# Kernel tuning notes

Hardware: AMD Instinct MI355X
Metric: run time of the kernel (lower is better)

The kernel has to match this reference:

```python
import jax, jax.numpy as jnp
import numpy as np
import math

B, N, FEAT, H, NONGT, M, POS = 16, 1024, 768, 8, 20, 10, 64
DG = FEAT // H  # per-head dim = 96
NEG = -9e15


def setup_inputs() -> dict:
    key = jax.random.key(0)
    ks = jax.random.split(key, 14)
    s = 0.02
    return dict(
        roi_feat=jax.random.normal(ks[0], (B, N, FEAT), jnp.float32),
        adj_matrix=jax.random.randint(ks[1], (B, N, NONGT), 0, 2).astype(jnp.int32),
        position_embedding=jax.random.uniform(ks[2], (B, N, NONGT, POS), jnp.float32),
        label_biases_att=jax.random.normal(ks[3], (B, N, NONGT), jnp.float32) * 0.1,
        aux_feat=jax.random.normal(ks[4], (B, 1, FEAT), jnp.float32),
        Wq=jax.random.normal(ks[5], (FEAT, FEAT), jnp.float32) * s,
        bq=jnp.zeros((FEAT,), jnp.float32),
        Wk=jax.random.normal(ks[6], (FEAT, FEAT), jnp.float32) * s,
        bk=jnp.zeros((FEAT,), jnp.float32),
        Wpos=jax.random.normal(ks[7], (POS, H), jnp.float32) * s,
        bpos=jnp.zeros((H,), jnp.float32),
        m_k=jax.random.normal(ks[8], (1, M, FEAT), jnp.float32) * (1.0 / FEAT / H),
        m_v=jax.random.normal(ks[9], (1, M, FEAT), jnp.float32) * (1.0 / M),
        Wout=jax.random.normal(ks[10], (H, DG, FEAT), jnp.float32) * s,  # grouped 1x1 conv: per-head [DG, FEAT]
        bout=jnp.zeros((FEAT,), jnp.float32),
    )


def reference(roi_feat, adj_matrix, position_embedding, label_biases_att, aux_feat,
              Wq, bq, Wk, bk, Wpos, bpos, m_k, m_v, Wout, bout):
    b, n, f = roi_feat.shape
    nongt = min(NONGT, n)
    nongt_feat = roi_feat[:, :nongt]                               # [B,nongt,F]

    q = (roi_feat @ Wq + bq).reshape(b, n, H, DG)                  # [B,N,H,DG]
    scale_m = math.sqrt(f / H)
    mk = scale_m * m_k * aux_feat                                  # [B,M,F] (broadcast)
    mv = scale_m * m_v * aux_feat                                  # [B,M,F]
    k = jnp.concatenate([nongt_feat @ Wk + bk, mk], axis=1)        # [B,K,F], K=nongt+M
    v = jnp.concatenate([nongt_feat, mv], axis=1)                  # [B,K,F]
    kk = k.reshape(b, nongt + M, H, DG)

    # scaled QK^T -> [B,N,H,K]
    aff = jnp.einsum('bnhd,bkhd->bnhk', q, kk) / math.sqrt(DG)

    # geometric position bias: log(max(relu(fc(pos)), 1e-6)) on first nongt keys
    pos = jax.nn.relu(position_embedding @ Wpos + bpos)            # [B,N,nongt,H]
    bias = jnp.log(jnp.maximum(pos, 1e-6))
    aff_n = aff[:, :, :, :nongt] + jnp.transpose(bias, (0, 1, 3, 2))

    # adjacency mask + label bias on first nongt keys
    mask = (adj_matrix > 0)[:, :, None, :]                         # [B,N,1,nongt]
    aff_n = jnp.where(mask, aff_n, NEG) + label_biases_att[:, :, None, :]

    weighted = jnp.concatenate([aff_n, aff[:, :, :, nongt:]], axis=-1)
    p = jax.nn.softmax(weighted, axis=-1)                          # [B,N,H,K]

    out_t = jnp.einsum('bnhk,bkf->bnhf', p, v)                     # [B,N,H,F]
    # weight-normed grouped 1x1 conv == per-head linear F -> DG, concat over heads
    out = jnp.einsum('bnhf,hgf->bnhg', out_t, Wout).reshape(b, n, f) + bout
    return out
```

## Files before the change

kernel.cpp:

```cpp
#include <hip/hip_runtime.h>
#include <hip/hip_bf16.h>
#include <cstdint>

typedef __bf16 bf16;
typedef __bf16 bf16x4 __attribute__((ext_vector_type(4)));
typedef __bf16 bf16x8 __attribute__((ext_vector_type(8)));
typedef float f32x4 __attribute__((ext_vector_type(4)));

#define B_ 16
#define N_ 1024
#define FEAT_ 768
#define H_ 8
#define NONGT_ 20
#define M_ 10
#define POS_ 64
#define DG_ 96
#define KTOT_ 30
#define KPAD_ 32
#define ROWS_ (B_*N_)
#define SCALE_M 9.797958971132712f
#define INV_SQRT_DG 0.10206207261596575f
#define NEG_ -9.0e15f

__device__ __forceinline__ void gload16(const void* g, void* lds) {
  __builtin_amdgcn_global_load_lds(
      (const __attribute__((address_space(1))) unsigned int*)g,
      (__attribute__((address_space(3))) unsigned int*)lds, 16, 0, 0);
}

__device__ __forceinline__ bf16x8 cvt8(float4 a, float4 b) {
  bf16x8 o;
  o[0]=(bf16)a.x; o[1]=(bf16)a.y; o[2]=(bf16)a.z; o[3]=(bf16)a.w;
  o[4]=(bf16)b.x; o[5]=(bf16)b.y; o[6]=(bf16)b.z; o[7]=(bf16)b.w;
  return o;
}

__global__ void prep_kernel(const float* __restrict__ Wq, const float* __restrict__ Wk,
                            const float* __restrict__ Wout, const float* __restrict__ roi,
                            const float* __restrict__ aux, const float* __restrict__ m_v,
                            const float* __restrict__ m_k,
                            bf16* __restrict__ Wq_t, bf16* __restrict__ Wk_t,
                            bf16* __restrict__ Whi, bf16* __restrict__ Wlo,
                            bf16* __restrict__ Vbf, bf16* __restrict__ kbuf,
                            bf16* __restrict__ Abf)
{
  int idx = blockIdx.x * blockDim.x + threadIdx.x;
  int stride = gridDim.x * blockDim.x;
  for (int i = idx; i < FEAT_*FEAT_; i += stride) {
    int n = i / FEAT_, k = i % FEAT_;
    Wq_t[i] = (bf16)Wq[k*FEAT_ + n];
    Wk_t[i] = (bf16)Wk[k*FEAT_ + n];
    float w = Wout[i];
    bf16 hi = (bf16)w;
    Whi[i] = hi;
    Wlo[i] = (bf16)(w - (float)hi);
  }
  for (int i = idx; i < B_*KPAD_*FEAT_; i += stride) {
    int f = i % FEAT_;
    int r = (i / FEAT_) % KPAD_;
    int b = i / (FEAT_*KPAD_);
    float v;
    if (r < NONGT_)      v = roi[((size_t)b*N_ + r)*FEAT_ + f];
    else if (r < KTOT_)  v = SCALE_M * m_v[(r-NONGT_)*FEAT_ + f] * aux[b*FEAT_ + f];
    else                 v = 0.f;
    Vbf[i] = (bf16)v;
  }
  for (int i = idx; i < B_*12*FEAT_; i += stride) {
    int f = i % FEAT_;
    int rr = (i / FEAT_) % 12;
    int b = i / (FEAT_*12);
    float v = (rr < M_) ? SCALE_M * m_k[rr*FEAT_ + f] * aux[b*FEAT_ + f] : 0.f;
    kbuf[((size_t)b*KPAD_ + NONGT_ + rr)*FEAT_ + f] = (bf16)v;
  }
  const int total8 = ROWS_*FEAT_/8;
  for (int i = idx; i < total8; i += stride) {
    const float4* p = (const float4*)(roi + (size_t)i*8);
    *(bf16x8*)(Abf + (size_t)i*8) = cvt8(p[0], p[1]);
  }
}

__global__ __launch_bounds__(256, 2) void gemm_fused_kernel(
    const bf16* __restrict__ A, const bf16* __restrict__ Wq_t,
    const float* __restrict__ bq, bf16* __restrict__ qbuf,
    const bf16* __restrict__ Wk_t, const bf16* __restrict__ Vbf,
    const bf16* __restrict__ Whi, const bf16* __restrict__ Wlo,
    const float* __restrict__ bk, bf16* __restrict__ kbuf,
    bf16* __restrict__ vwT_hi, bf16* __restrict__ vwT_lo)
{
  __shared__ __align__(16) bf16 sA[128*32];
  __shared__ __align__(16) bf16 sB[128*32];
  const int tid = threadIdx.x;
  const int w = tid >> 6, l = tid & 63;
  const int bx = blockIdx.x;
  const int fr = l & 15, fq = l >> 4, fko = fq << 3;

  if (bx < 768) {
    const int x = bx & 7, j = bx >> 3;
    const int mbase = (x + 8*(j/6)) * 128;
    const int nbase = (j % 6) * 128;
    const int wr = w >> 1, wc = w & 1;
    const int srow = tid >> 2;
    const int scol = (tid & 3) << 3;
    const bf16* Ag0 = A + (size_t)(mbase + srow)*FEAT_ + scol;
    const bf16* Ag1 = Ag0 + (size_t)64*FEAT_;
    const bf16* Bg0 = Wq_t + (size_t)(nbase + srow)*FEAT_ + scol;
    const bf16* Bg1 = Bg0 + (size_t)64*FEAT_;
    bf16* ldsA0 = sA + w*512;
    bf16* ldsA1 = sA + 2048 + w*512;
    bf16* ldsB0 = sB + w*512;
    bf16* ldsB1 = sB + 2048 + w*512;
    f32x4 acc[4][4] = {};
    for (int kt = 0; kt < FEAT_/32; ++kt) {
      __syncthreads();
      gload16(Ag0 + kt*32, ldsA0);
      gload16(Ag1 + kt*32, ldsA1);
      gload16(Bg0 + kt*32, ldsB0);
      gload16(Bg1 + kt*32, ldsB1);
      __syncthreads();
      bf16x8 af[4], bff[4];
      #pragma unroll
      for (int m = 0; m < 4; ++m)
        af[m] = *(const bf16x8*)(sA + (wr*64 + m*16 + fr)*32 + fko);
      #pragma unroll
      for (int n = 0; n < 4; ++n)
        bff[n] = *(const bf16x8*)(sB + (wc*64 + n*16 + fr)*32 + fko);
      #pragma unroll
      for (int m = 0; m < 4; ++m) {
        #pragma unroll
        for (int n = 0; n < 4; ++n)
          acc[m][n] = __builtin_amdgcn_mfma_f32_16x16x32_bf16(af[m], bff[n], acc[m][n], 0, 0, 0);
      }
    }
    #pragma unroll
    for (int n = 0; n < 4; ++n) {
      const int col = nbase + wc*64 + n*16 + fr;
      const float bv = bq[col];
      #pragma unroll
      for (int m = 0; m < 4; ++m) {
        const int row = mbase + wr*64 + m*16 + fq*4;
        #pragma unroll
        for (int r = 0; r < 4; ++r)
          qbuf[(size_t)(row + r)*FEAT_ + col] = (bf16)(acc[m][n][r] + bv);
      }
    }
  } else {
    const int widx = (bx - 768)*4 + w;
    const int cbase = (widx % 48) * 16;
    const int by = widx / 48;
    f32x4 acc = {};
    if (by < 32) {
      const bf16* Ap = A + ((size_t)(by >> 1)*N_ + (by & 1)*16 + fr)*FEAT_ + fko;
      const bf16* Bp = Wk_t + (size_t)(cbase + fr)*FEAT_ + fko;
      #pragma unroll
      for (int kt = 0; kt < FEAT_/32; ++kt) {
        bf16x8 a = *(const bf16x8*)(Ap + kt*32);
        bf16x8 b = *(const bf16x8*)(Bp + kt*32);
        acc = __builtin_amdgcn_mfma_f32_16x16x32_bf16(a, b, acc, 0, 0, 0);
      }
      const float bv = bk[cbase + fr];
      #pragma unroll
      for (int r = 0; r < 4; ++r) {
        const int rl = (by & 1)*16 + fq*4 + r;
        if (rl < NONGT_)
          kbuf[((size_t)(by >> 1)*KPAD_ + rl)*FEAT_ + cbase + fr] = (bf16)(acc[r] + bv);
      }
    } else {
      const int rt = by - 32;
      const bf16* Ap = Vbf + ((size_t)rt*16 + fr)*FEAT_ + fko;
      const bf16* B1 = Whi + (size_t)(cbase + fr)*FEAT_ + fko;
      const bf16* B2 = Wlo + (size_t)(cbase + fr)*FEAT_ + fko;
      f32x4 acc2 = {};
      #pragma unroll
      for (int kt = 0; kt < FEAT_/32; ++kt) {
        bf16x8 a = *(const bf16x8*)(Ap + kt*32);
        acc  = __builtin_amdgcn_mfma_f32_16x16x32_bf16(a, *(const bf16x8*)(B1 + kt*32), acc,  0, 0, 0);
        acc2 = __builtin_amdgcn_mfma_f32_16x16x32_bf16(a, *(const bf16x8*)(B2 + kt*32), acc2, 0, 0, 0);
      }
      #pragma unroll
      for (int r = 0; r < 4; ++r) {
        const int grow = rt*16 + fq*4 + r;
        const int b = grow >> 5, key = grow & 31;
        float vv = acc[r] + acc2[r];
        bf16 vh = (bf16)vv;
        size_t addr = ((size_t)b*FEAT_ + cbase + fr)*KPAD_ + key;
        vwT_hi[addr] = vh;
        vwT_lo[addr] = (bf16)(vv - (float)vh);
      }
    }
  }
}

__global__ __launch_bounds__(64, 4) void posbias_kernel(
    const float* __restrict__ pe, const float* __restrict__ Wpos,
    const float* __restrict__ bpos, float* __restrict__ posb)
{
  __shared__ __align__(16) float spe[NONGT_*68];
  __shared__ __align__(16) float swpT[H_*68];
  __shared__ float sbp[H_];
  const int row = blockIdx.x;
  const int l = threadIdx.x;
  const float* per = pe + (size_t)row*NONGT_*POS_;
  for (int i = l; i < NONGT_*POS_; i += 64) spe[(i >> 6)*68 + (i & 63)] = per[i];
  for (int i = l; i < POS_*H_; i += 64) swpT[(i & 7)*68 + (i >> 3)] = Wpos[i];
  if (l < H_) sbp[l] = bpos[l];
  __syncthreads();
  #pragma unroll
  for (int t = 0; t < 3; ++t) {
    int idx = t*64 + l;
    if (idx < NONGT_*H_) {
      int j = idx >> 3, h = idx & 7;
      float s = sbp[h];
      const float4* a4 = (const float4*)(spe + j*68);
      const float4* b4 = (const float4*)(swpT + h*68);
      #pragma unroll
      for (int p4 = 0; p4 < 16; ++p4) {
        float4 a = a4[p4], bv = b4[p4];
        s += a.x*bv.x + a.y*bv.y + a.z*bv.z + a.w*bv.w;
      }
      s = fmaxf(s, 0.f);
      posb[(size_t)row*160 + h*20 + j] = __logf(fmaxf(s, 1e-6f));
    }
  }
}

__global__ __launch_bounds__(256, 4) void attn_kernel(
    const bf16* __restrict__ qbuf, const bf16* __restrict__ kbuf,
    const bf16* __restrict__ vwT_hi, const bf16* __restrict__ vwT_lo,
    const float* __restrict__ posb, const int* __restrict__ adj,
    const float* __restrict__ lb, const float* __restrict__ bout,
    float* __restrict__ out)
{
  __shared__ __align__(16) bf16 sph[H_*16*40];
  __shared__ __align__(16) bf16 spl[H_*16*40];
  const int tid = threadIdx.x;
  const int w = tid >> 6, l = tid & 63;
  const int fr = l & 15, fq = l >> 4, fko = fq << 3;
  const int row0 = blockIdx.x * 16;
  const int b = blockIdx.y;
  const size_t rabs = (size_t)b*N_ + row0 + fr;

  #pragma unroll
  for (int hi2 = 0; hi2 < 2; ++hi2) {
    const int h = w*2 + hi2;
    const bf16* kp = kbuf + (size_t)b*KPAD_*FEAT_ + h*DG_ + fko;
    const bf16* qp = qbuf + rabs*FEAT_ + h*DG_ + fko;
    f32x4 acc0 = {}, acc1 = {};
    #pragma unroll
    for (int kt = 0; kt < 3; ++kt) {
      bf16x8 qa = *(const bf16x8*)(qp + kt*32);
      bf16x8 k0 = *(const bf16x8*)(kp + (size_t)fr*FEAT_ + kt*32);
      bf16x8 k1 = *(const bf16x8*)(kp + (size_t)(16 + fr)*FEAT_ + kt*32);
      acc0 = __builtin_amdgcn_mfma_f32_16x16x32_bf16(k0, qa, acc0, 0, 0, 0);
      acc1 = __builtin_amdgcn_mfma_f32_16x16x32_bf16(k1, qa, acc1, 0, 0, 0);
    }
    const float* pbr = posb + rabs*160 + h*20;
    const int*   adjr = adj + rabs*20;
    const float* lbr  = lb  + rabs*20;
    float lg[2][4];
    #pragma unroll
    for (int r = 0; r < 4; ++r) {
      int j0 = fq*4 + r;
      float v0 = acc0[r] * INV_SQRT_DG;
      v0 = (adjr[j0] > 0 ? v0 + pbr[j0] : NEG_) + lbr[j0];
      lg[0][r] = v0;
      int j1 = 16 + fq*4 + r;
      float v1 = acc1[r] * INV_SQRT_DG;
      if (j1 < NONGT_)      v1 = (adjr[j1] > 0 ? v1 + pbr[j1] : NEG_) + lbr[j1];
      else if (j1 >= KTOT_) v1 = -3.0e38f;
      lg[1][r] = v1;
    }
    float m = lg[0][0];
    #pragma unroll
    for (int jt = 0; jt < 2; ++jt)
      #pragma unroll
      for (int r = 0; r < 4; ++r) m = fmaxf(m, lg[jt][r]);
    m = fmaxf(m, __shfl_xor(m, 16));
    m = fmaxf(m, __shfl_xor(m, 32));
    float s = 0.f;
    float e[2][4];
    #pragma unroll
    for (int jt = 0; jt < 2; ++jt)
      #pragma unroll
      for (int r = 0; r < 4; ++r) { e[jt][r] = __expf(lg[jt][r] - m); s += e[jt][r]; }
    s += __shfl_xor(s, 16);
    s += __shfl_xor(s, 32);
    const float inv = 1.f / s;
    #pragma unroll
    for (int jt = 0; jt < 2; ++jt) {
      bf16x4 ph, pl;
      #pragma unroll
      for (int r = 0; r < 4; ++r) {
        float p = e[jt][r] * inv;
        ph[r] = (bf16)p;
        pl[r] = (bf16)(p - (float)ph[r]);
      }
      const int off = (h*16 + fr)*40 + jt*16 + fq*4;
      *(bf16x4*)(sph + off) = ph;
      *(bf16x4*)(spl + off) = pl;
    }
    bf16x8 pa_h = *(const bf16x8*)(sph + (h*16 + fr)*40 + fko);
    bf16x8 pa_l = *(const bf16x8*)(spl + (h*16 + fr)*40 + fko);
    #pragma unroll
    for (int ct = 0; ct < 6; ++ct) {
      const int col = h*DG_ + ct*16 + fr;
      const size_t vaddr = ((size_t)b*FEAT_ + col)*KPAD_ + fko;
      bf16x8 vh = *(const bf16x8*)(vwT_hi + vaddr);
      bf16x8 vl = *(const bf16x8*)(vwT_lo + vaddr);
      f32x4 o = {};
      o = __builtin_amdgcn_mfma_f32_16x16x32_bf16(pa_h, vh, o, 0, 0, 0);
      o = __builtin_amdgcn_mfma_f32_16x16x32_bf16(pa_h, vl, o, 0, 0, 0);
      o = __builtin_amdgcn_mfma_f32_16x16x32_bf16(pa_l, vh, o, 0, 0, 0);
      const float bv = bout[col];
      #pragma unroll
      for (int r = 0; r < 4; ++r)
        out[((size_t)b*N_ + row0 + fq*4 + r)*FEAT_ + col] = o[r] + bv;
    }
  }
}

extern "C" void kernel_launch(void* const* d_in, const int* in_sizes, int n_in,
                              void* d_out, int out_size, void* d_ws, size_t ws_size,
                              hipStream_t stream) {
  const float* roi  = (const float*)d_in[0];
  const int*   adj  = (const int*)  d_in[1];
  const float* pe   = (const float*)d_in[2];
  const float* lb   = (const float*)d_in[3];
  const float* aux  = (const float*)d_in[4];
  const float* Wq   = (const float*)d_in[5];
  const float* bq   = (const float*)d_in[6];
  const float* Wk   = (const float*)d_in[7];
  const float* bk   = (const float*)d_in[8];
  const float* Wpos = (const float*)d_in[9];
  const float* bpos = (const float*)d_in[10];
  const float* m_k  = (const float*)d_in[11];
  const float* m_v  = (const float*)d_in[12];
  const float* Wout = (const float*)d_in[13];
  const float* bout = (const float*)d_in[14];
  float* out = (float*)d_out;

  char* pw = (char*)d_ws;
  auto carve = [&](size_t bytes) -> void* {
    void* r = pw; pw += (bytes + 255) & ~(size_t)255; return r;
  };
  bf16*  Abf    = (bf16*) carve((size_t)ROWS_*FEAT_*2);
  bf16*  qbuf   = (bf16*) carve((size_t)ROWS_*FEAT_*2);
  bf16*  Wq_t   = (bf16*) carve((size_t)FEAT_*FEAT_*2);
  bf16*  Wk_t   = (bf16*) carve((size_t)FEAT_*FEAT_*2);
  bf16*  Whi    = (bf16*) carve((size_t)FEAT_*FEAT_*2);
  bf16*  Wlo    = (bf16*) carve((size_t)FEAT_*FEAT_*2);
  bf16*  Vbf    = (bf16*) carve((size_t)B_*KPAD_*FEAT_*2);
  bf16*  kbuf   = (bf16*) carve((size_t)B_*KPAD_*FEAT_*2);
  bf16*  vwT_hi = (bf16*) carve((size_t)B_*FEAT_*KPAD_*2);
  bf16*  vwT_lo = (bf16*) carve((size_t)B_*FEAT_*KPAD_*2);
  float* posb   = (float*)carve((size_t)ROWS_*160*4);

  posbias_kernel<<<dim3(16384), dim3(64), 0, stream>>>(pe, Wpos, bpos, posb);
  prep_kernel<<<dim3(2048), dim3(256), 0, stream>>>(Wq, Wk, Wout, roi, aux, m_v, m_k,
                                                    Wq_t, Wk_t, Whi, Wlo, Vbf, kbuf, Abf);
  gemm_fused_kernel<<<dim3(1536), dim3(256), 0, stream>>>(Abf, Wq_t, bq, qbuf,
                                                          Wk_t, Vbf, Whi, Wlo, bk, kbuf,
                                                          vwT_hi, vwT_lo);
  attn_kernel<<<dim3(64, 16), dim3(256), 0, stream>>>(qbuf, kbuf, vwT_hi, vwT_lo,
                                                      posb, adj, lb, bout, out);
}
```

Baseline: 133.1 us.

## Fuse fp32-to-bf16 conversion of roi into GEMM with double-buffered LDS pipeline

Drops the separate pass that converted roi_feat to a bf16 copy. The Q and K GEMMs now read fp32 roi directly and convert in registers, saving a full write and re-read of a 25 MB buffer. The Q GEMM main loop is restructured into a double-buffered LDS pipeline: the next tile's A values are prefetched into registers and its B values via global_load_lds while the current tile's MFMAs run, leaving one barrier per iteration. The Wq/Wk transposes in prep now read coalesced and write strided, and the prep grid is halved. In exchange the GEMM reads twice as many bytes for A and doubles its LDS use, which may reduce occupancy.

Result: faster. 127.6 us (-4.2%).

```diff
diff --git a/kernel.cpp b/kernel.cpp
--- a/kernel.cpp
+++ b/kernel.cpp
@@ -41,15 +41,15 @@
                             const float* __restrict__ m_k,
                             bf16* __restrict__ Wq_t, bf16* __restrict__ Wk_t,
                             bf16* __restrict__ Whi, bf16* __restrict__ Wlo,
-                            bf16* __restrict__ Vbf, bf16* __restrict__ kbuf,
-                            bf16* __restrict__ Abf)
+                            bf16* __restrict__ Vbf, bf16* __restrict__ kbuf)
 {
   int idx = blockIdx.x * blockDim.x + threadIdx.x;
   int stride = gridDim.x * blockDim.x;
   for (int i = idx; i < FEAT_*FEAT_; i += stride) {
-    int n = i / FEAT_, k = i % FEAT_;
-    Wq_t[i] = (bf16)Wq[k*FEAT_ + n];
-    Wk_t[i] = (bf16)Wk[k*FEAT_ + n];
+    int k = i / FEAT_, n = i % FEAT_;
+    bf16 q = (bf16)Wq[i], kk = (bf16)Wk[i];
+    Wq_t[(size_t)n*FEAT_ + k] = q;
+    Wk_t[(size_t)n*FEAT_ + k] = kk;
     float w = Wout[i];
     bf16 hi = (bf16)w;
     Whi[i] = hi;
@@ -72,23 +72,18 @@
     float v = (rr < M_) ? SCALE_M * m_k[rr*FEAT_ + f] * aux[b*FEAT_ + f] : 0.f;
     kbuf[((size_t)b*KPAD_ + NONGT_ + rr)*FEAT_ + f] = (bf16)v;
   }
-  const int total8 = ROWS_*FEAT_/8;
-  for (int i = idx; i < total8; i += stride) {
-    const float4* p = (const float4*)(roi + (size_t)i*8);
-    *(bf16x8*)(Abf + (size_t)i*8) = cvt8(p[0], p[1]);
-  }
 }
 
 __global__ __launch_bounds__(256, 2) void gemm_fused_kernel(
-    const bf16* __restrict__ A, const bf16* __restrict__ Wq_t,
+    const float* __restrict__ roi, const bf16* __restrict__ Wq_t,
     const float* __restrict__ bq, bf16* __restrict__ qbuf,
     const bf16* __restrict__ Wk_t, const bf16* __restrict__ Vbf,
     const bf16* __restrict__ Whi, const bf16* __restrict__ Wlo,
     const float* __restrict__ bk, bf16* __restrict__ kbuf,
     bf16* __restrict__ vwT_hi, bf16* __restrict__ vwT_lo)
 {
-  __shared__ __align__(16) bf16 sA[128*32];
-  __shared__ __align__(16) bf16 sB[128*32];
+  __shared__ __align__(16) bf16 sA[2*128*32];
+  __shared__ __align__(16) bf16 sB[2*128*32];
   const int tid = threadIdx.x;
   const int w = tid >> 6, l = tid & 63;
   const int bx = blockIdx.x;
@@ -101,35 +96,50 @@
     const int wr = w >> 1, wc = w & 1;
     const int srow = tid >> 2;
     const int scol = (tid & 3) << 3;
-    const bf16* Ag0 = A + (size_t)(mbase + srow)*FEAT_ + scol;
-    const bf16* Ag1 = Ag0 + (size_t)64*FEAT_;
-    const bf16* Bg0 = Wq_t + (size_t)(nbase + srow)*FEAT_ + scol;
-    const bf16* Bg1 = Bg0 + (size_t)64*FEAT_;
-    bf16* ldsA0 = sA + w*512;
-    bf16* ldsA1 = sA + 2048 + w*512;
-    bf16* ldsB0 = sB + w*512;
-    bf16* ldsB1 = sB + 2048 + w*512;
+    const float* Ag0 = roi + (size_t)(mbase + srow)*FEAT_ + scol;
+    const float* Ag1 = Ag0 + (size_t)64*FEAT_;
+    const bf16*  Bg0 = Wq_t + (size_t)(nbase + srow)*FEAT_ + scol;
+    const bf16*  Bg1 = Bg0 + (size_t)64*FEAT_;
     f32x4 acc[4][4] = {};
-    for (int kt = 0; kt < FEAT_/32; ++kt) {
+    {
+      float4 a00 = *(const float4*)Ag0, a01 = *(const float4*)(Ag0 + 4);
+      float4 a10 = *(const float4*)Ag1, a11 = *(const float4*)(Ag1 + 4);
+      gload16(Bg0, sB + w*512);
+      gload16(Bg1, sB + 2048 + w*512);
+      *(bf16x8*)(sA + srow*32 + scol) = cvt8(a00, a01);
+      *(bf16x8*)(sA + (64 + srow)*32 + scol) = cvt8(a10, a11);
       __syncthreads();
-      gload16(Ag0 + kt*32, ldsA0);
-      gload16(Ag1 + kt*32, ldsA1);
-      gload16(Bg0 + kt*32, ldsB0);
-      gload16(Bg1 + kt*32, ldsB1);
-      __syncthreads();
+    }
+    for (int kt = 0; kt < 24; ++kt) {
+      const int cur = (kt & 1) << 12;
+      const int nxt = ((kt + 1) & 1) << 12;
+      float4 p00, p01, p10, p11;
+      if (kt < 23) {
+        const float* An0 = Ag0 + (kt + 1)*32;
+        const float* An1 = Ag1 + (kt + 1)*32;
+        p00 = *(const float4*)An0; p01 = *(const float4*)(An0 + 4);
+        p10 = *(const float4*)An1; p11 = *(const float4*)(An1 + 4);
+        gload16(Bg0 + (kt + 1)*32, sB + nxt + w*512);
+        gload16(Bg1 + (kt + 1)*32, sB + nxt + 2048 + w*512);
+      }
       bf16x8 af[4], bff[4];
       #pragma unroll
       for (int m = 0; m < 4; ++m)
-        af[m] = *(const bf16x8*)(sA + (wr*64 + m*16 + fr)*32 + fko);
+        af[m] = *(const bf16x8*)(sA + cur + (wr*64 + m*16 + fr)*32 + fko);
       #pragma unroll
       for (int n = 0; n < 4; ++n)
-        bff[n] = *(const bf16x8*)(sB + (wc*64 + n*16 + fr)*32 + fko);
+        bff[n] = *(const bf16x8*)(sB + cur + (wc*64 + n*16 + fr)*32 + fko);
       #pragma unroll
       for (int m = 0; m < 4; ++m) {
         #pragma unroll
         for (int n = 0; n < 4; ++n)
           acc[m][n] = __builtin_amdgcn_mfma_f32_16x16x32_bf16(af[m], bff[n], acc[m][n], 0, 0, 0);
       }
+      if (kt < 23) {
+        *(bf16x8*)(sA + nxt + srow*32 + scol) = cvt8(p00, p01);
+        *(bf16x8*)(sA + nxt + (64 + srow)*32 + scol) = cvt8(p10, p11);
+      }
+      __syncthreads();
     }
     #pragma unroll
     for (int n = 0; n < 4; ++n) {
@@ -149,13 +159,14 @@
     const int by = widx / 48;
     f32x4 acc = {};
     if (by < 32) {
-      const bf16* Ap = A + ((size_t)(by >> 1)*N_ + (by & 1)*16 + fr)*FEAT_ + fko;
+      const float* Ap = roi + ((size_t)(by >> 1)*N_ + (by & 1)*16 + fr)*FEAT_ + fko;
       const bf16* Bp = Wk_t + (size_t)(cbase + fr)*FEAT_ + fko;
       #pragma unroll
       for (int kt = 0; kt < FEAT_/32; ++kt) {
-        bf16x8 a = *(const bf16x8*)(Ap + kt*32);
+        float4 a0 = *(const float4*)(Ap + kt*32);
+        float4 a1 = *(const float4*)(Ap + kt*32 + 4);
         bf16x8 b = *(const bf16x8*)(Bp + kt*32);
-        acc = __builtin_amdgcn_mfma_f32_16x16x32_bf16(a, b, acc, 0, 0, 0);
+        acc = __builtin_amdgcn_mfma_f32_16x16x32_bf16(cvt8(a0, a1), b, acc, 0, 0, 0);
       }
       const float bv = bk[cbase + fr];
       #pragma unroll
@@ -342,7 +353,6 @@
   auto carve = [&](size_t bytes) -> void* {
     void* r = pw; pw += (bytes + 255) & ~(size_t)255; return r;
   };
-  bf16*  Abf    = (bf16*) carve((size_t)ROWS_*FEAT_*2);
   bf16*  qbuf   = (bf16*) carve((size_t)ROWS_*FEAT_*2);
   bf16*  Wq_t   = (bf16*) carve((size_t)FEAT_*FEAT_*2);
   bf16*  Wk_t   = (bf16*) carve((size_t)FEAT_*FEAT_*2);
@@ -355,9 +365,9 @@
   float* posb   = (float*)carve((size_t)ROWS_*160*4);
 
   posbias_kernel<<<dim3(16384), dim3(64), 0, stream>>>(pe, Wpos, bpos, posb);
-  prep_kernel<<<dim3(2048), dim3(256), 0, stream>>>(Wq, Wk, Wout, roi, aux, m_v, m_k,
-                                                    Wq_t, Wk_t, Whi, Wlo, Vbf, kbuf, Abf);
-  gemm_fused_kernel<<<dim3(1536), dim3(256), 0, stream>>>(Abf, Wq_t, bq, qbuf,
+  prep_kernel<<<dim3(1024), dim3(256), 0, stream>>>(Wq, Wk, Wout, roi, aux, m_v, m_k,
+                                                    Wq_t, Wk_t, Whi, Wlo, Vbf, kbuf);
+  gemm_fused_kernel<<<dim3(1536), dim3(256), 0, stream>>>(roi, Wq_t, bq, qbuf,
                                                           Wk_t, Vbf, Whi, Wlo, bk, kbuf,
                                                           vwT_hi, vwT_lo);
   attn_kernel<<<dim3(64, 16), dim3(256), 0, stream>>>(qbuf, kbuf, vwT_hi, vwT_lo,
```
